# Kernel tuning notes

Hardware: AMD Instinct MI355X
Metric: run time of the kernel (lower is better)

The kernel has to match this reference:

```python
import math
import jax, jax.numpy as jnp
import numpy as np

EMBED = 512
HEADS = 2
HEAD_DIM = EMBED // HEADS


def setup_inputs() -> dict:
    key = jax.random.key(0)
    ks = jax.random.split(key, 10)
    s = 1.0 / math.sqrt(EMBED)
    return {
        "text_embeds": jax.random.normal(ks[0], (64, 32, EMBED), jnp.float32),
        "video_embeds": jax.random.normal(ks[1], (128, 64, EMBED), jnp.float32),
        "Wq": jax.random.normal(ks[2], (EMBED, EMBED), jnp.float32) * s,
        "bq": jnp.zeros((EMBED,), jnp.float32),
        "Wk": jax.random.normal(ks[3], (EMBED, EMBED), jnp.float32) * s,
        "bk": jnp.zeros((EMBED,), jnp.float32),
        "Wv": jax.random.normal(ks[4], (EMBED, EMBED), jnp.float32) * s,
        "bv": jnp.zeros((EMBED,), jnp.float32),
        "Wo": jax.random.normal(ks[5], (EMBED, EMBED), jnp.float32) * s,
        "bo": jnp.zeros((EMBED,), jnp.float32),
    }


def reference(text_embeds, video_embeds, Wq, bq, Wk, bk, Wv, bv, Wo, bo):
    num_texts, num_words, _ = text_embeds.shape
    num_vids, num_frames, _ = video_embeds.shape
    # projections (torch Linear: x @ W.T + b)
    q = (text_embeds @ Wq.T + bq).reshape(num_texts, num_words, HEADS, HEAD_DIM)
    k = (video_embeds @ Wk.T + bk).reshape(num_vids, num_frames, HEADS, HEAD_DIM)
    v = (video_embeds @ Wv.T + bv).reshape(num_vids, num_frames, HEADS, HEAD_DIM)
    # 5D cross attention logits: [vids, texts, heads, frames, words]
    logits = jnp.einsum('avhd,bthd->abhvt', k, q) / math.sqrt(HEAD_DIM)
    weights = jax.nn.softmax(logits, axis=3)  # softmax over frames
    attn = jnp.einsum('avhd,abhvt->abhtd', v, weights)  # [a,b,h,t,d]
    # faithful to torch: reshape (a,b,h,t,d) -> (a,b,t,h*d) in row-major order
    attn = attn.reshape(num_vids, num_texts, num_words, EMBED)
    attn = attn.mean(axis=0)  # [texts, words, embed]
    return attn @ Wo.T + bo
```

## Files before the change

### kernel.cpp

```cpp
#include <hip/hip_runtime.h>
#include <hip/hip_bf16.h>
#include <math.h>

#define EMBED  512
#define HEADS  2
#define HDIM   256
#define NTEXT  64
#define NWORD  32
#define NVID   128
#define NFRM   64

typedef __attribute__((ext_vector_type(8))) short      short8;
typedef __attribute__((ext_vector_type(8))) unsigned short ushort8;
typedef __attribute__((ext_vector_type(4))) float      float4v;
typedef __attribute__((ext_vector_type(4))) unsigned short ushort4v;

__device__ __forceinline__ unsigned short f2bf(float x) {
    __hip_bfloat16 h = __float2bfloat16(x);
    return *(unsigned short*)&h;
}
__device__ __forceinline__ float bf2f(unsigned short u) {
    __hip_bfloat16 h = *(__hip_bfloat16*)&u;
    return __bfloat162float(h);
}

__device__ __forceinline__ void gload_lds16(unsigned short* dst, const unsigned short* src) {
#if __has_builtin(__builtin_amdgcn_global_load_lds)
    __builtin_amdgcn_global_load_lds((const __attribute__((address_space(1))) void*)src,
                                     (__attribute__((address_space(3))) void*)dst,
                                     16, 0, 0);
#else
    *(ushort8*)dst = *(const ushort8*)src;
#endif
}

__global__ __launch_bounds__(256)
void cvt5(const float* __restrict__ s0, const float* __restrict__ s1,
          const float* __restrict__ s2, const float* __restrict__ s3,
          const float* __restrict__ s4, unsigned short* __restrict__ dst) {
    const int y = blockIdx.y;
    const float* s; size_t off; int n4;
    if (y == 0)      { s = s0; off = 0;       n4 = 262144;  }
    else if (y == 1) { s = s1; off = 1048576; n4 = 1048576; }
    else if (y == 2) { s = s2; off = 5242880; n4 = 65536;   }
    else if (y == 3) { s = s3; off = 5505024; n4 = 65536;   }
    else             { s = s4; off = 5767168; n4 = 65536;   }
    unsigned short* d = dst + off;
    for (int i = blockIdx.x * 256 + threadIdx.x; i < n4; i += 512 * 256) {
        float4v f = ((const float4v*)s)[i];
        ((ushort4v*)d)[i] = (ushort4v){f2bf(f.x), f2bf(f.y), f2bf(f.z), f2bf(f.w)};
    }
}

__global__ __launch_bounds__(256)
void proj_qkv(const unsigned short* __restrict__ text, const unsigned short* __restrict__ video,
              const unsigned short* __restrict__ Wqb, const float* __restrict__ bq,
              const unsigned short* __restrict__ Wkb, const float* __restrict__ bk,
              const unsigned short* __restrict__ Wvb, const float* __restrict__ bv,
              unsigned short* __restrict__ qout,
              unsigned short* __restrict__ Kgf, unsigned short* __restrict__ Vgf) {
    const int mb = blockIdx.x, nb = blockIdx.y;
    const int bj = nb * 128;
    const unsigned short *A, *W;
    const float* bias;
    int op, arow0, abase = 0;
    if (mb < 16)      { op = 0; A = text;  W = Wqb; bias = bq; arow0 = mb * 128; }
    else if (mb < 80) { op = 1; A = video; W = Wkb; bias = bk; abase = (mb - 16) * 2; arow0 = abase * 64; }
    else              { op = 2; A = video; W = Wvb; bias = bv; abase = (mb - 80) * 2; arow0 = abase * 64; }

    __shared__ __align__(16) unsigned char smem[65536];

    const int tid = threadIdx.x;
    const int w = tid >> 6, lane = tid & 63;
    const int lm = lane & 15, qd = lane >> 4;
    const int wr = w >> 1, wc = w & 1;

    float4v acc[4][4];
    #pragma unroll
    for (int rt = 0; rt < 4; ++rt)
        #pragma unroll
        for (int ct = 0; ct < 4; ++ct) acc[rt][ct] = (float4v){0.f, 0.f, 0.f, 0.f};

    auto STAGE = [&](int buf, int k0) {
        unsigned short* AbL = (unsigned short*)(smem + buf * 32768);
        unsigned short* WbL = (unsigned short*)(smem + buf * 32768 + 16384);
        #pragma unroll
        for (int it = 0; it < 4; ++it) {
            const int s = tid + it * 256;
            const int r = s >> 3, c8 = s & 7;
            const int sc = (c8 ^ (r & 7)) * 8;
            gload_lds16(&AbL[(size_t)s * 8], &A[(size_t)(arow0 + r) * 512 + k0 + sc]);
            gload_lds16(&WbL[(size_t)s * 8], &W[(size_t)(bj    + r) * 512 + k0 + sc]);
        }
    };

    STAGE(0, 0);
    __syncthreads();
    int cur = 0;
    for (int ks = 0; ks < 8; ++ks) {
        if (ks < 7) STAGE(cur ^ 1, (ks + 1) * 64);
        const unsigned short* AbL = (const unsigned short*)(smem + cur * 32768);
        const unsigned short* WbL = (const unsigned short*)(smem + cur * 32768 + 16384);
        #pragma unroll
        for (int kq = 0; kq < 2; ++kq) {
            const int scol = (kq * 32 + qd * 8) ^ ((lm & 7) * 8);
            short8 af[4], bf[4];
            #pragma unroll
            for (int rt = 0; rt < 4; ++rt)
                af[rt] = *(const short8*)&AbL[(wr * 64 + rt * 16 + lm) * 64 + scol];
            #pragma unroll
            for (int ct = 0; ct < 4; ++ct)
                bf[ct] = *(const short8*)&WbL[(wc * 64 + ct * 16 + lm) * 64 + scol];
            #pragma unroll
            for (int rt = 0; rt < 4; ++rt)
                #pragma unroll
                for (int ct = 0; ct < 4; ++ct)
                    acc[rt][ct] = __builtin_amdgcn_mfma_f32_16x16x32_bf16(af[rt], bf[ct], acc[rt][ct], 0, 0, 0);
        }
        __syncthreads();
        cur ^= 1;
    }

    if (op == 0) {
        #pragma unroll
        for (int rt = 0; rt < 4; ++rt)
            #pragma unroll
            for (int ct = 0; ct < 4; ++ct) {
                const int c = bj + wc * 64 + ct * 16 + lm;
                const float bb = bias[c];
                #pragma unroll
                for (int reg = 0; reg < 4; ++reg) {
                    const int r = arow0 + wr * 64 + rt * 16 + qd * 4 + reg;
                    qout[(size_t)r * 512 + c] = f2bf((acc[rt][ct][reg] + bb) * 0.0625f);
                }
            }
        return;
    }

    const int a   = abase + wr;
    const int bjs = bj + wc * 64;
    const int h      = bjs >> 8;
    const int bj_rel = bjs & 255;
    unsigned short (*Eb)[72] = (unsigned short (*)[72])(smem + w * 9216);
    const size_t base = ((size_t)(h * 128 + a)) * 16384;

    if (op == 1) {
        #pragma unroll
        for (int ct = 0; ct < 4; ++ct) {
            const int dl = ct * 16 + lm;
            const float bb = bias[bjs + dl];
            #pragma unroll
            for (int rt = 0; rt < 4; ++rt)
                #pragma unroll
                for (int reg = 0; reg < 4; ++reg)
                    Eb[rt * 16 + qd * 4 + reg][dl] = f2bf(acc[rt][ct][reg] + bb);
        }
        __syncthreads();
        #pragma unroll
        for (int it = 0; it < 8; ++it) {
            const int s = lane + it * 64;
            const int ntf = s >> 7, kqr = (s >> 6) & 1, l = s & 63;
            const int v = ntf * 16 + (l & 15);
            const int dl = kqr * 32 + (l >> 4) * 8;
            ushort8 val = *(const ushort8*)&Eb[v][dl];
            *(ushort8*)&Kgf[base + ((size_t)(ntf * 8 + (bj_rel >> 5) + kqr) * 64 + l) * 8] = val;
        }
    } else {
        #pragma unroll
        for (int ct = 0; ct < 4; ++ct) {
            const int dl = ct * 16 + lm;
            const float bb = bias[bjs + dl];
            #pragma unroll
            for (int rt = 0; rt < 4; ++rt)
                #pragma unroll
                for (int reg = 0; reg < 4; ++reg)
                    Eb[dl][rt * 16 + qd * 4 + reg] = f2bf(acc[rt][ct][reg] + bb);
        }
        __syncthreads();
        #pragma unroll
        for (int it = 0; it < 8; ++it) {
            const int s = lane + it * 64;
            const int ntr = s >> 7, kqv = (s >> 6) & 1, l = s & 63;
            const int dl = ntr * 16 + (l & 15);
            const int v0 = kqv * 32 + (l >> 4) * 8;
            ushort8 val = *(const ushort8*)&Eb[dl][v0];
            *(ushort8*)&Vgf[base + ((size_t)(((bj_rel >> 4) + ntr) * 2 + kqv) * 64 + l) * 8] = val;
        }
    }
}

__global__ __launch_bounds__(512, 2)
void attn9(const unsigned short* __restrict__ Kgf,
           const unsigned short* __restrict__ Vgf,
           const unsigned short* __restrict__ q,
           unsigned short* __restrict__ partg) {
    const int c  = blockIdx.x;
    const int h  = blockIdx.y;
    const int tg = blockIdx.z;
    const int tid = threadIdx.x;
    const int w = tid >> 6, lane = tid & 63;
    const int lm = lane & 15, qd = lane >> 4;
    const int wt = w >> 1;
    const int fh = w & 1;
    const int b = tg * 4 + wt;

    __shared__ __align__(16) unsigned short Kb[2][16384];
    __shared__ __align__(16) unsigned short Vb[2][16384];
    __shared__ __align__(16) unsigned short Pf[4][2][2][512];
    __shared__ __align__(16) float Ex[4][2][2][16][2];

    short8 qf[2][8];
    #pragma unroll
    for (int mt = 0; mt < 2; ++mt)
        #pragma unroll
        for (int kq = 0; kq < 8; ++kq)
            qf[mt][kq] = *(const short8*)
                &q[((size_t)(b * 32 + mt * 16 + lm)) * 512 + h * 256 + kq * 32 + qd * 8];

    float4v pacc[2][8];
    #pragma unroll
    for (int mt = 0; mt < 2; ++mt)
        #pragma unroll
        for (int nd = 0; nd < 8; ++nd) pacc[mt][nd] = (float4v){0.f, 0.f, 0.f, 0.f};

    const size_t vb0 = (size_t)(h * 128 + c * 16) * 16384;

    #pragma unroll
    for (int i = 0; i < 4; ++i) {
        const int s = tid + i * 512;
        gload_lds16(&Kb[0][(size_t)s * 8], &Kgf[vb0 + (size_t)s * 8]);
        gload_lds16(&Vb[0][(size_t)s * 8], &Vgf[vb0 + (size_t)s * 8]);
    }
    #pragma unroll
    for (int i = 0; i < 4; ++i) {
        const int s = tid + i * 512;
        gload_lds16(&Kb[1][(size_t)s * 8], &Kgf[vb0 + 16384 + (size_t)s * 8]);
        gload_lds16(&Vb[1][(size_t)s * 8], &Vgf[vb0 + 16384 + (size_t)s * 8]);
    }
    __syncthreads();

    for (int ai = 0; ai < 16; ++ai) {
        const int cur = ai & 1;

        float4v lacc[2][2];
        #pragma unroll
        for (int nt = 0; nt < 2; ++nt)
            #pragma unroll
            for (int mt = 0; mt < 2; ++mt) lacc[nt][mt] = (float4v){0.f, 0.f, 0.f, 0.f};
        #pragma unroll
        for (int kq = 0; kq < 8; ++kq) {
            #pragma unroll
            for (int nt = 0; nt < 2; ++nt) {
                const short8 kf = *(const short8*)
                    &Kb[cur][(((fh * 2 + nt) * 8 + kq) * 64 + lane) * 8];
                lacc[nt][0] = __builtin_amdgcn_mfma_f32_16x16x32_bf16(kf, qf[0][kq], lacc[nt][0], 0, 0, 0);
                lacc[nt][1] = __builtin_amdgcn_mfma_f32_16x16x32_bf16(kf, qf[1][kq], lacc[nt][1], 0, 0, 0);
            }
        }

        float m2[2], sv[2], e[2][2][4];
        #pragma unroll
        for (int mt = 0; mt < 2; ++mt) {
            float mm = lacc[0][mt][0];
            #pragma unroll
            for (int nt = 0; nt < 2; ++nt)
                #pragma unroll
                for (int r = 0; r < 4; ++r) mm = fmaxf(mm, lacc[nt][mt][r]);
            mm = fmaxf(mm, __shfl_xor(mm, 16));
            mm = fmaxf(mm, __shfl_xor(mm, 32));
            float ss = 0.f;
            #pragma unroll
            for (int nt = 0; nt < 2; ++nt)
                #pragma unroll
                for (int r = 0; r < 4; ++r) {
                    const float ev = __expf(lacc[nt][mt][r] - mm);
                    e[mt][nt][r] = ev;
                    ss += ev;
                }
            ss += __shfl_xor(ss, 16);
            ss += __shfl_xor(ss, 32);
            m2[mt] = mm; sv[mt] = ss;
            if (qd == 0) {
                Ex[wt][fh][mt][lm][0] = mm;
                Ex[wt][fh][mt][lm][1] = ss;
            }
        }
        __syncthreads();

        #pragma unroll
        for (int mt = 0; mt < 2; ++mt) {
            const float om = Ex[wt][fh ^ 1][mt][lm][0];
            const float os = Ex[wt][fh ^ 1][mt][lm][1];
            const float M   = fmaxf(m2[mt], om);
            const float den = sv[mt] * __expf(m2[mt] - M) + os * __expf(om - M);
            const float fac = __expf(m2[mt] - M) / den;
            #pragma unroll
            for (int nt = 0; nt < 2; ++nt) {
                ushort4v pv;
                pv.x = f2bf(e[mt][nt][0] * fac);
                pv.y = f2bf(e[mt][nt][1] * fac);
                pv.z = f2bf(e[mt][nt][2] * fac);
                pv.w = f2bf(e[mt][nt][3] * fac);
                *(ushort4v*)&Pf[wt][mt][fh][(lm + 16 * (nt * 2 + (qd >> 1))) * 8 + (qd & 1) * 4] = pv;
            }
        }
        __syncthreads();

        #pragma unroll
        for (int kqv = 0; kqv < 2; ++kqv) {
            const short8 pf0 = *(const short8*)&Pf[wt][0][kqv][lane * 8];
            const short8 pf1 = *(const short8*)&Pf[wt][1][kqv][lane * 8];
            #pragma unroll
            for (int nd = 0; nd < 8; ++nd) {
                const short8 vf = *(const short8*)
                    &Vb[cur][(((fh * 8 + nd) * 2 + kqv) * 64 + lane) * 8];
                pacc[0][nd] = __builtin_amdgcn_mfma_f32_16x16x32_bf16(pf0, vf, pacc[0][nd], 0, 0, 0);
                pacc[1][nd] = __builtin_amdgcn_mfma_f32_16x16x32_bf16(pf1, vf, pacc[1][nd], 0, 0, 0);
            }
        }
        __syncthreads();

        if (ai < 14) {
            const size_t kb = vb0 + (size_t)(ai + 2) * 16384;
            #pragma unroll
            for (int i = 0; i < 4; ++i) {
                const int s = tid + i * 512;
                gload_lds16(&Kb[cur][(size_t)s * 8], &Kgf[kb + (size_t)s * 8]);
                gload_lds16(&Vb[cur][(size_t)s * 8], &Vgf[kb + (size_t)s * 8]);
            }
        }
    }

    unsigned short* part = partg + (size_t)c * 1048576;
    #pragma unroll
    for (int mt = 0; mt < 2; ++mt)
        #pragma unroll
        for (int nd = 0; nd < 8; ++nd)
            #pragma unroll
            for (int r = 0; r < 4; ++r) {
                const int t = mt * 16 + qd * 4 + r;
                const int d = fh * 128 + nd * 16 + lm;
                const int row = b * 32 + h * 16 + (t >> 1);
                const int col = (t & 1) * 256 + d;
                part[(size_t)row * 512 + col] = f2bf(pacc[mt][nd][r]);
            }
}

__global__ __launch_bounds__(256)
void reduce8(unsigned short* __restrict__ partg) {
    const size_t i = ((size_t)blockIdx.x * 256 + threadIdx.x) * 8;
    float s[8];
    #pragma unroll
    for (int j = 0; j < 8; ++j) s[j] = 0.f;
    #pragma unroll
    for (int p = 0; p < 8; ++p) {
        ushort8 u = *(const ushort8*)&partg[(size_t)p * 1048576 + i];
        #pragma unroll
        for (int j = 0; j < 8; ++j) s[j] += bf2f(u[j]);
    }
    ushort8 o;
    #pragma unroll
    for (int j = 0; j < 8; ++j) o[j] = f2bf(s[j] * 0.0078125f);
    *(ushort8*)&partg[i] = o;
}

__global__ __launch_bounds__(256)
void proj_o(const unsigned short* __restrict__ Abf, const float* __restrict__ W,
            const float* __restrict__ bias, float* __restrict__ C) {
    __shared__ __align__(16) unsigned short Ab[64][72];
    __shared__ __align__(16) unsigned short Wb[64][72];
    const int tid = threadIdx.x;
    const int bi = blockIdx.x * 64, bj = blockIdx.y * 64;
    const int w = tid >> 6, lane = tid & 63;
    const int lm = lane & 15, qd = lane >> 4;

    float4v acc[4];
    #pragma unroll
    for (int nt = 0; nt < 4; ++nt) acc[nt] = (float4v){0.f, 0.f, 0.f, 0.f};

    for (int k0 = 0; k0 < 512; k0 += 64) {
        #pragma unroll
        for (int it = 0; it < 2; ++it) {
            const int s = tid + it * 256;
            const int r = s >> 3, c8 = (s & 7) * 8;
            *(ushort8*)&Ab[r][c8] = *(const ushort8*)&Abf[(size_t)(bi + r) * 512 + k0 + c8];
        }
        #pragma unroll
        for (int it = 0; it < 4; ++it) {
            const int s = tid + it * 256;
            const int r = s >> 4, c4 = (s & 15) * 4;
            float4v fw = *(const float4v*)&W[(size_t)(bj + r) * 512 + k0 + c4];
            *(ushort4v*)&Wb[r][c4] = (ushort4v){f2bf(fw.x), f2bf(fw.y), f2bf(fw.z), f2bf(fw.w)};
        }
        __syncthreads();
        #pragma unroll
        for (int kq = 0; kq < 2; ++kq) {
            const short8 af = *(const short8*)&Ab[w * 16 + lm][kq * 32 + qd * 8];
            #pragma unroll
            for (int nt = 0; nt < 4; ++nt) {
                const short8 bf = *(const short8*)&Wb[nt * 16 + lm][kq * 32 + qd * 8];
                acc[nt] = __builtin_amdgcn_mfma_f32_16x16x32_bf16(af, bf, acc[nt], 0, 0, 0);
            }
        }
        __syncthreads();
    }
    #pragma unroll
    for (int nt = 0; nt < 4; ++nt) {
        const int cc = bj + nt * 16 + lm;
        const float bb = bias[cc];
        #pragma unroll
        for (int reg = 0; reg < 4; ++reg) {
            const int r = bi + w * 16 + qd * 4 + reg;
            C[(size_t)r * 512 + cc] = acc[nt][reg] + bb;
        }
    }
}

extern "C" void kernel_launch(void* const* d_in, const int* in_sizes, int n_in,
                              void* d_out, int out_size, void* d_ws, size_t ws_size,
                              hipStream_t stream) {
    const float* text  = (const float*)d_in[0];
    const float* video = (const float*)d_in[1];
    const float* Wq = (const float*)d_in[2];
    const float* bq = (const float*)d_in[3];
    const float* Wk = (const float*)d_in[4];
    const float* bk = (const float*)d_in[5];
    const float* Wv = (const float*)d_in[6];
    const float* bv = (const float*)d_in[7];
    const float* Wo = (const float*)d_in[8];
    const float* bo = (const float*)d_in[9];

    unsigned short* Kgf   = (unsigned short*)d_ws;
    unsigned short* Vgf   = (unsigned short*)((char*)d_ws + (8u << 20));
    unsigned short* partg = (unsigned short*)((char*)d_ws + (16u << 20));
    unsigned short* textbf  = partg;
    unsigned short* videobf = partg + 1048576;
    unsigned short* wqbf    = partg + 5242880;
    unsigned short* wkbf    = partg + 5505024;
    unsigned short* wvbf    = partg + 5767168;
    unsigned short* qbf   = (unsigned short*)d_out;
    float*          out   = (float*)d_out;

    cvt5<<<dim3(512, 5), 256, 0, stream>>>(text, video, Wq, Wk, Wv, partg);
    proj_qkv<<<dim3(144, 4), 256, 0, stream>>>(textbf, videobf, wqbf, bq, wkbf, bk,
                                               wvbf, bv, qbf, Kgf, Vgf);
    attn9<<<dim3(8, 2, 16), 512, 0, stream>>>(Kgf, Vgf, qbf, partg);
    reduce8<<<dim3(512), 256, 0, stream>>>(partg);
    proj_o<<<dim3(32, 8), 256, 0, stream>>>(partg, Wo, bo, out);
}
```

Before: 167.1 us.

## Remap attention warps so each K/V fragment serves two texts

Reassigns the eight warps in the attention kernel. Each warp now handles two texts and a quarter of the frames and head dimension, where before it handled one text and half of the frames and head dimension. Every K and V fragment loaded from shared memory now feeds four MFMAs instead of two, halving LDS reads per MFMA. The cost is a softmax reduction across four warps instead of two through shared memory, more Q fragments held in registers, and possible register pressure under the (512,2) launch bounds.

```diff
diff --git a/kernel.cpp b/kernel.cpp
--- a/kernel.cpp
+++ b/kernel.cpp
@@ -190,38 +190,42 @@
 }
 
 __global__ __launch_bounds__(512, 2)
-void attn9(const unsigned short* __restrict__ Kgf,
-           const unsigned short* __restrict__ Vgf,
-           const unsigned short* __restrict__ q,
-           unsigned short* __restrict__ partg) {
+void attn11(const unsigned short* __restrict__ Kgf,
+            const unsigned short* __restrict__ Vgf,
+            const unsigned short* __restrict__ q,
+            unsigned short* __restrict__ partg) {
     const int c  = blockIdx.x;
     const int h  = blockIdx.y;
     const int tg = blockIdx.z;
     const int tid = threadIdx.x;
     const int w = tid >> 6, lane = tid & 63;
     const int lm = lane & 15, qd = lane >> 4;
-    const int wt = w >> 1;
-    const int fh = w & 1;
-    const int b = tg * 4 + wt;
+    const int sub = w >> 1;
+    const int wp  = w & 1;
 
     __shared__ __align__(16) unsigned short Kb[2][16384];
     __shared__ __align__(16) unsigned short Vb[2][16384];
     __shared__ __align__(16) unsigned short Pf[4][2][2][512];
-    __shared__ __align__(16) float Ex[4][2][2][16][2];
-
-    short8 qf[2][8];
-    #pragma unroll
-    for (int mt = 0; mt < 2; ++mt)
-        #pragma unroll
-        for (int kq = 0; kq < 8; ++kq)
-            qf[mt][kq] = *(const short8*)
-                &q[((size_t)(b * 32 + mt * 16 + lm)) * 512 + h * 256 + kq * 32 + qd * 8];
-
-    float4v pacc[2][8];
-    #pragma unroll
-    for (int mt = 0; mt < 2; ++mt)
-        #pragma unroll
-        for (int nd = 0; nd < 8; ++nd) pacc[mt][nd] = (float4v){0.f, 0.f, 0.f, 0.f};
+    __shared__ __align__(16) float Ex[2][4][4][16][2];
+
+    short8 qf[2][2][8];
+    #pragma unroll
+    for (int tx = 0; tx < 2; ++tx)
+        #pragma unroll
+        for (int mt = 0; mt < 2; ++mt)
+            #pragma unroll
+            for (int kq = 0; kq < 8; ++kq)
+                qf[tx][mt][kq] = *(const short8*)
+                    &q[((size_t)((tg * 4 + wp * 2 + tx) * 32 + mt * 16 + lm)) * 512
+                       + h * 256 + kq * 32 + qd * 8];
+
+    float4v pacc[2][2][4];
+    #pragma unroll
+    for (int tx = 0; tx < 2; ++tx)
+        #pragma unroll
+        for (int mt = 0; mt < 2; ++mt)
+            #pragma unroll
+            for (int nd = 0; nd < 4; ++nd) pacc[tx][mt][nd] = (float4v){0.f, 0.f, 0.f, 0.f};
 
     const size_t vb0 = (size_t)(h * 128 + c * 16) * 16384;
 
@@ -244,78 +248,87 @@
 
         float4v lacc[2][2];
         #pragma unroll
-        for (int nt = 0; nt < 2; ++nt)
-            #pragma unroll
-            for (int mt = 0; mt < 2; ++mt) lacc[nt][mt] = (float4v){0.f, 0.f, 0.f, 0.f};
+        for (int tx = 0; tx < 2; ++tx)
+            #pragma unroll
+            for (int mt = 0; mt < 2; ++mt) lacc[tx][mt] = (float4v){0.f, 0.f, 0.f, 0.f};
         #pragma unroll
         for (int kq = 0; kq < 8; ++kq) {
-            #pragma unroll
-            for (int nt = 0; nt < 2; ++nt) {
-                const short8 kf = *(const short8*)
-                    &Kb[cur][(((fh * 2 + nt) * 8 + kq) * 64 + lane) * 8];
-                lacc[nt][0] = __builtin_amdgcn_mfma_f32_16x16x32_bf16(kf, qf[0][kq], lacc[nt][0], 0, 0, 0);
-                lacc[nt][1] = __builtin_amdgcn_mfma_f32_16x16x32_bf16(kf, qf[1][kq], lacc[nt][1], 0, 0, 0);
-            }
-        }
-
-        float m2[2], sv[2], e[2][2][4];
-        #pragma unroll
-        for (int mt = 0; mt < 2; ++mt) {
-            float mm = lacc[0][mt][0];
-            #pragma unroll
-            for (int nt = 0; nt < 2; ++nt)
-                #pragma unroll
-                for (int r = 0; r < 4; ++r) mm = fmaxf(mm, lacc[nt][mt][r]);
-            mm = fmaxf(mm, __shfl_xor(mm, 16));
-            mm = fmaxf(mm, __shfl_xor(mm, 32));
-            float ss = 0.f;
-            #pragma unroll
-            for (int nt = 0; nt < 2; ++nt)
+            const short8 kf = *(const short8*)&Kb[cur][((sub * 8 + kq) * 64 + lane) * 8];
+            #pragma unroll
+            for (int tx = 0; tx < 2; ++tx)
+                #pragma unroll
+                for (int mt = 0; mt < 2; ++mt)
+                    lacc[tx][mt] = __builtin_amdgcn_mfma_f32_16x16x32_bf16(kf, qf[tx][mt][kq], lacc[tx][mt], 0, 0, 0);
+        }
+
+        float m1[2][2], e[2][2][4];
+        #pragma unroll
+        for (int tx = 0; tx < 2; ++tx)
+            #pragma unroll
+            for (int mt = 0; mt < 2; ++mt) {
+                float mm = lacc[tx][mt][0];
+                #pragma unroll
+                for (int r = 1; r < 4; ++r) mm = fmaxf(mm, lacc[tx][mt][r]);
+                mm = fmaxf(mm, __shfl_xor(mm, 16));
+                mm = fmaxf(mm, __shfl_xor(mm, 32));
+                float ss = 0.f;
                 #pragma unroll
                 for (int r = 0; r < 4; ++r) {
-                    const float ev = __expf(lacc[nt][mt][r] - mm);
-                    e[mt][nt][r] = ev;
+                    const float ev = __expf(lacc[tx][mt][r] - mm);
+                    e[tx][mt][r] = ev;
                     ss += ev;
                 }
-            ss += __shfl_xor(ss, 16);
-            ss += __shfl_xor(ss, 32);
-            m2[mt] = mm; sv[mt] = ss;
-            if (qd == 0) {
-                Ex[wt][fh][mt][lm][0] = mm;
-                Ex[wt][fh][mt][lm][1] = ss;
-            }
-        }
-        __syncthreads();
-
-        #pragma unroll
-        for (int mt = 0; mt < 2; ++mt) {
-            const float om = Ex[wt][fh ^ 1][mt][lm][0];
-            const float os = Ex[wt][fh ^ 1][mt][lm][1];
-            const float M   = fmaxf(m2[mt], om);
-            const float den = sv[mt] * __expf(m2[mt] - M) + os * __expf(om - M);
-            const float fac = __expf(m2[mt] - M) / den;
-            #pragma unroll
-            for (int nt = 0; nt < 2; ++nt) {
+                ss += __shfl_xor(ss, 16);
+                ss += __shfl_xor(ss, 32);
+                m1[tx][mt] = mm;
+                if (qd == 0) {
+                    Ex[wp][sub][tx * 2 + mt][lm][0] = mm;
+                    Ex[wp][sub][tx * 2 + mt][lm][1] = ss;
+                }
+            }
+        __syncthreads();
+
+        #pragma unroll
+        for (int tx = 0; tx < 2; ++tx)
+            #pragma unroll
+            for (int mt = 0; mt < 2; ++mt) {
+                const int wi = tx * 2 + mt;
+                float M = Ex[wp][0][wi][lm][0];
+                M = fmaxf(M, Ex[wp][1][wi][lm][0]);
+                M = fmaxf(M, Ex[wp][2][wi][lm][0]);
+                M = fmaxf(M, Ex[wp][3][wi][lm][0]);
+                float den = 0.f;
+                #pragma unroll
+                for (int ftp = 0; ftp < 4; ++ftp)
+                    den += Ex[wp][ftp][wi][lm][1] * __expf(Ex[wp][ftp][wi][lm][0] - M);
+                const float fac = __expf(m1[tx][mt] - M) / den;
                 ushort4v pv;
-                pv.x = f2bf(e[mt][nt][0] * fac);
-                pv.y = f2bf(e[mt][nt][1] * fac);
-                pv.z = f2bf(e[mt][nt][2] * fac);
-                pv.w = f2bf(e[mt][nt][3] * fac);
-                *(ushort4v*)&Pf[wt][mt][fh][(lm + 16 * (nt * 2 + (qd >> 1))) * 8 + (qd & 1) * 4] = pv;
-            }
-        }
+                pv.x = f2bf(e[tx][mt][0] * fac);
+                pv.y = f2bf(e[tx][mt][1] * fac);
+                pv.z = f2bf(e[tx][mt][2] * fac);
+                pv.w = f2bf(e[tx][mt][3] * fac);
+                *(ushort4v*)&Pf[wp * 2 + tx][mt][sub >> 1]
+                    [(lm + 16 * ((sub & 1) * 2 + (qd >> 1))) * 8 + (qd & 1) * 4] = pv;
+            }
         __syncthreads();
 
         #pragma unroll
         for (int kqv = 0; kqv < 2; ++kqv) {
-            const short8 pf0 = *(const short8*)&Pf[wt][0][kqv][lane * 8];
-            const short8 pf1 = *(const short8*)&Pf[wt][1][kqv][lane * 8];
-            #pragma unroll
-            for (int nd = 0; nd < 8; ++nd) {
+            short8 pf[2][2];
+            #pragma unroll
+            for (int tx = 0; tx < 2; ++tx)
+                #pragma unroll
+                for (int mt = 0; mt < 2; ++mt)
+                    pf[tx][mt] = *(const short8*)&Pf[wp * 2 + tx][mt][kqv][lane * 8];
+            #pragma unroll
+            for (int nd = 0; nd < 4; ++nd) {
                 const short8 vf = *(const short8*)
-                    &Vb[cur][(((fh * 8 + nd) * 2 + kqv) * 64 + lane) * 8];
-                pacc[0][nd] = __builtin_amdgcn_mfma_f32_16x16x32_bf16(pf0, vf, pacc[0][nd], 0, 0, 0);
-                pacc[1][nd] = __builtin_amdgcn_mfma_f32_16x16x32_bf16(pf1, vf, pacc[1][nd], 0, 0, 0);
+                    &Vb[cur][(((sub * 4 + nd) * 2 + kqv) * 64 + lane) * 8];
+                #pragma unroll
+                for (int tx = 0; tx < 2; ++tx)
+                    #pragma unroll
+                    for (int mt = 0; mt < 2; ++mt)
+                        pacc[tx][mt][nd] = __builtin_amdgcn_mfma_f32_16x16x32_bf16(pf[tx][mt], vf, pacc[tx][mt][nd], 0, 0, 0);
             }
         }
         __syncthreads();
@@ -333,17 +346,22 @@
 
     unsigned short* part = partg + (size_t)c * 1048576;
     #pragma unroll
-    for (int mt = 0; mt < 2; ++mt)
-        #pragma unroll
-        for (int nd = 0; nd < 8; ++nd)
-            #pragma unroll
-            for (int r = 0; r < 4; ++r) {
-                const int t = mt * 16 + qd * 4 + r;
-                const int d = fh * 128 + nd * 16 + lm;
-                const int row = b * 32 + h * 16 + (t >> 1);
-                const int col = (t & 1) * 256 + d;
-                part[(size_t)row * 512 + col] = f2bf(pacc[mt][nd][r]);
-            }
+    for (int tx = 0; tx < 2; ++tx) {
+        const int b = tg * 4 + wp * 2 + tx;
+        #pragma unroll
+        for (int mt = 0; mt < 2; ++mt)
+            #pragma unroll
+            for (int nd = 0; nd < 4; ++nd) {
+                const int d = sub * 64 + nd * 16 + lm;
+                #pragma unroll
+                for (int r = 0; r < 4; ++r) {
+                    const int t = mt * 16 + qd * 4 + r;
+                    const int row = b * 32 + h * 16 + (t >> 1);
+                    const int col = (t & 1) * 256 + d;
+                    part[(size_t)row * 512 + col] = f2bf(pacc[tx][mt][nd][r]);
+                }
+            }
+    }
 }
 
 __global__ __launch_bounds__(256)
@@ -444,7 +462,7 @@
     cvt5<<<dim3(512, 5), 256, 0, stream>>>(text, video, Wq, Wk, Wv, partg);
     proj_qkv<<<dim3(144, 4), 256, 0, stream>>>(textbf, videobf, wqbf, bq, wkbf, bk,
                                                wvbf, bv, qbf, Kgf, Vgf);
-    attn9<<<dim3(8, 2, 16), 512, 0, stream>>>(Kgf, Vgf, qbf, partg);
+    attn11<<<dim3(8, 2, 16), 512, 0, stream>>>(Kgf, Vgf, qbf, partg);
     reduce8<<<dim3(512), 256, 0, stream>>>(partg);
     proj_o<<<dim3(32, 8), 256, 0, stream>>>(partg, Wo, bo, out);
 }
```

After: 187.3 us. +12.1%, slower.
